# Kernel optimization log

Measured on AMD Instinct MI355X. Metric: run time of the kernel, lower is better.

The kernel has to match this reference:

```python
import jax, jax.numpy as jnp
import numpy as np

H = 32          # total heads
K = 8           # active heads per token
D = 128         # head_dim = embed_dim // active_heads
E = 1024        # embed_dim
S = 1024        # seq_len
MAX_SEQ = 8192
BASE = 10000.0
SCALE = D ** -0.5
LB_W = 0.01
ENT_W = 0.01


def _rope(v, cos, sin):
    # v: (T, D); cos/sin: (T, D)
    v1, v2 = v[:, : D // 2], v[:, D // 2:]
    rot = jnp.concatenate([-v2, v1], axis=-1)
    return v * cos + rot * sin


def setup_inputs() -> dict:
    key = jax.random.key(0)
    ks = jax.random.split(key, 6)
    x = jax.random.normal(ks[0], (1, S, E), jnp.float32)
    Wq = jax.random.normal(ks[1], (E, H * D), jnp.float32) * 0.02
    Wk = jax.random.normal(ks[2], (E, H * D), jnp.float32) * 0.02
    Wv = jax.random.normal(ks[3], (E, H * D), jnp.float32) * 0.02
    Wr = jax.random.normal(ks[4], (E, H), jnp.float32) * 0.02
    Wo = jax.random.normal(ks[5], (K * D, E), jnp.float32) * 0.02
    head_counts = jnp.zeros((1, H), jnp.int32)
    return {"x": x, "Wq": Wq, "Wk": Wk, "Wv": Wv, "Wr": Wr, "Wo": Wo,
            "head_counts": head_counts}


def reference(x, Wq, Wk, Wv, Wr, Wo, head_counts):
    # ---- routing (eval mode: no gumbel noise) ----
    logits = x @ Wr                                   # (1, S, H)
    soft_probs = jax.nn.softmax(logits, axis=-1)
    top_logits, head_idx = jax.lax.top_k(logits, K)   # (1, S, K)
    head_w = jax.nn.softmax(top_logits, axis=-1)      # (1, S, K)

    # ---- aux loss ----
    primary = head_idx[..., 0]                        # (1, S)
    one_hot_p = jax.nn.one_hot(primary, H, dtype=jnp.float32)
    f = one_hot_p.mean(axis=1)                        # (1, H)
    p = soft_probs.mean(axis=1)                       # (1, H)
    balance = H * (f * p).sum(axis=-1).mean()
    entropy = -(soft_probs * jnp.log(soft_probs + 1e-8)).sum(axis=-1)
    entropy_loss = -entropy.mean()
    z_loss = (jax.nn.logsumexp(logits, axis=-1) ** 2).mean() * 0.01
    aux_loss = LB_W * balance + ENT_W * entropy_loss + z_loss

    # ---- projections + per-token gather of selected heads ----
    q_all = (x @ Wq).reshape(1, S, H, D)
    k_all = (x @ Wk).reshape(1, S, H, D)
    v_all = (x @ Wv).reshape(1, S, H, D)
    gidx = head_idx[..., None]                        # (1, S, K, 1)
    q = jnp.take_along_axis(q_all, gidx, axis=2)[0].reshape(S * K, D)
    k = jnp.take_along_axis(k_all, gidx, axis=2)[0].reshape(S * K, D)
    v = jnp.take_along_axis(v_all, gidx, axis=2)[0].reshape(S * K, D)

    heads_flat = head_idx[0].reshape(S * K)           # (T,)

    # rank of each dispatched token within its head (exclusive prefix count)
    oh = jax.nn.one_hot(heads_flat, H, dtype=jnp.int32)   # (T, H)
    excl = jnp.cumsum(oh, axis=0) - oh
    rank = jnp.take_along_axis(excl, heads_flat[:, None], axis=1)[:, 0]
    positions = rank + head_counts[0, heads_flat]
    positions = jnp.clip(positions, 0, MAX_SEQ - 1)

    # ---- per-head RoPE with per-head position counters ----
    inv_freq = 1.0 / (BASE ** (jnp.arange(0, D, 2, dtype=jnp.float32) / D))
    freqs = positions.astype(jnp.float32)[:, None] * inv_freq[None, :]
    emb = jnp.concatenate([freqs, freqs], axis=-1)    # (T, D)
    cos, sin = jnp.cos(emb), jnp.sin(emb)
    q = _rope(q, cos, sin)
    k = _rope(k, cos, sin)

    # ---- block-diagonal-causal attention (same head, earlier dispatch order) ----
    idx = jnp.arange(S * K)
    mask = (heads_flat[:, None] == heads_flat[None, :]) & (idx[None, :] <= idx[:, None])
    scores = (q @ k.T) * SCALE                        # (T, T)
    scores = jnp.where(mask, scores, jnp.float32(-1e30))
    attn = jax.nn.softmax(scores, axis=-1)
    out = attn @ v                                    # (T, D)

    # ---- combine with routing weights + output projection ----
    out = out.reshape(S, K, D) * head_w[0][..., None]
    out = out.reshape(S, K * D) @ Wo                  # (S, E)
    output = out[None]                                # (1, S, E)

    updated_counts = head_counts + oh.sum(axis=0)[None]
    return output, updated_counts, aux_loss
```

## Files before the change

kernel.cpp:

```cpp
#include <hip/hip_runtime.h>
#include <math.h>

#define S 1024
#define E 1024
#define H 32
#define KSEL 8
#define D 128
#define HD 4096
#define SK 8192
#define MAXL 1024
#define CAP 9216
#define ATTN_SCALE 0.08838834764831845f
#define SSTR 36
#define PSTR 40

#define NROUTER 256
#define NCONV 64
#define NTAB 512

typedef _Float16 half8 __attribute__((ext_vector_type(8)));
typedef _Float16 half4 __attribute__((ext_vector_type(4)));
typedef float floatx16 __attribute__((ext_vector_type(16)));
typedef float f4 __attribute__((ext_vector_type(4)));

#define GLOAD_LDS16(gsrc, ldst) \
    __builtin_amdgcn_global_load_lds( \
        (const __attribute__((address_space(1))) void*)(gsrc), \
        (__attribute__((address_space(3))) void*)(ldst), 16, 0, 0)

__global__ __launch_bounds__(256) void router_conv_kernel(
    const float* __restrict__ x, const float* __restrict__ Wr,
    int* __restrict__ head_idx, float* __restrict__ head_w,
    float* __restrict__ pbuf, float* __restrict__ entz,
    _Float16* __restrict__ xh,
    const float* __restrict__ Wo, _Float16* __restrict__ Wot,
    float2* __restrict__ tab)
{
    int bid = blockIdx.x, tid = threadIdx.x;
    if (bid >= NROUTER + NCONV) {
        int base = (bid - NROUTER - NCONV) * 1024;
        #pragma unroll
        for (int j = 0; j < 4; ++j) {
            int idx = base + j * 256 + tid;
            int p = idx >> 6, d2 = idx & 63;
            float inv = exp2f((float)d2 * -0.20762050f);
            float ang = (float)p * inv;
            float sn, cs;
            sincosf(ang, &sn, &cs);
            tab[idx] = make_float2(cs, sn);
        }
        return;
    }
    if (bid >= NROUTER) {
        __shared__ _Float16 tl[128 * 128];
        int cb = bid - NROUTER;
        int c0 = (cb & 7) * 128, r0 = (cb >> 3) * 128;
        #pragma unroll
        for (int p = 0; p < 16; ++p) {
            int idx = p * 256 + tid;
            int rr = idx >> 5, cg = (idx & 31) * 4;
            f4 v = *(const f4*)&Wo[(size_t)(r0 + rr) * 1024 + c0 + cg];
            half4 o;
            o.x = (_Float16)v.x; o.y = (_Float16)v.y;
            o.z = (_Float16)v.z; o.w = (_Float16)v.w;
            int sc = cg ^ (((rr >> 3) & 7) << 2);
            *(half4*)&tl[rr * 128 + sc] = o;
        }
        __syncthreads();
        #pragma unroll
        for (int p = 0; p < 8; ++p) {
            int chunk = p * 256 + tid;
            int cc = chunk >> 4, ch = chunk & 15;
            int cidx = cc ^ ((ch & 7) << 2);
            half8 o;
            #pragma unroll
            for (int j = 0; j < 8; ++j)
                o[j] = tl[(ch * 8 + j) * 128 + cidx];
            *(half8*)&Wot[(size_t)(c0 + cc) * 1024 + r0 + ch * 8] = o;
        }
        return;
    }
    int s = bid * 4 + (tid >> 6);
    int lane = tid & 63;
    int h = lane & 31, half = lane >> 5;
    const float* xr = x + (size_t)s * E + half * 512;
    const float* wr = Wr + (size_t)(half * 512) * H + h;
    float a0 = 0.f, a1 = 0.f, a2 = 0.f, a3 = 0.f;
    #pragma unroll 4
    for (int e = 0; e < 512; e += 4) {
        a0 += xr[e]     * wr[e * H];
        a1 += xr[e + 1] * wr[(e + 1) * H];
        a2 += xr[e + 2] * wr[(e + 2) * H];
        a3 += xr[e + 3] * wr[(e + 3) * H];
    }
    float acc = (a0 + a1) + (a2 + a3);
    acc += __shfl_xor(acc, 32, 64);
    float logit = acc;
    float m = logit;
    #pragma unroll
    for (int off = 16; off; off >>= 1) m = fmaxf(m, __shfl_xor(m, off, 64));
    float ex = expf(logit - m);
    float Z = ex;
    #pragma unroll
    for (int off = 16; off; off >>= 1) Z += __shfl_xor(Z, off, 64);
    float p = ex / Z;
    float es = p * logf(p + 1e-8f);
    #pragma unroll
    for (int off = 16; off; off >>= 1) es += __shfl_xor(es, off, 64);
    float lse = m + logf(Z);
    float lv = logit;
    float tv[KSEL]; int ti[KSEL];
    #pragma unroll
    for (int j = 0; j < KSEL; ++j) {
        float bv = lv; int bi = h;
        #pragma unroll
        for (int off = 16; off; off >>= 1) {
            float ov = __shfl_xor(bv, off, 64);
            int oi = __shfl_xor(bi, off, 64);
            if (ov > bv || (ov == bv && oi < bi)) { bv = ov; bi = oi; }
        }
        tv[j] = bv; ti[j] = bi;
        if (h == bi) lv = -INFINITY;
    }
    float Z2 = 0.f;
    #pragma unroll
    for (int j = 0; j < KSEL; ++j) Z2 += expf(tv[j] - tv[0]);
    if (lane < 32) pbuf[s * 32 + lane] = p;
    if (lane == 0) {
        entz[s * 2]     = es;
        entz[s * 2 + 1] = lse * lse;
        #pragma unroll
        for (int j = 0; j < KSEL; ++j) {
            head_idx[s * KSEL + j] = ti[j];
            head_w[s * KSEL + j]   = expf(tv[j] - tv[0]) / Z2;
        }
    }
    const float* xrow = x + (size_t)s * E;
    _Float16* xhrow = xh + (size_t)s * E;
    #pragma unroll
    for (int t = 0; t < 4; ++t) {
        int e = t * 256 + lane * 4;
        f4 v = *(const f4*)&xrow[e];
        half4 o;
        o.x = (_Float16)v.x; o.y = (_Float16)v.y; o.z = (_Float16)v.z; o.w = (_Float16)v.w;
        *(half4*)&xhrow[e] = o;
    }
}

__global__ __launch_bounds__(256) void scan_aux_kernel(
    const int* __restrict__ head_idx, const int* __restrict__ head_counts,
    int* __restrict__ order, int* __restrict__ hlen, float* __restrict__ out_counts,
    const float* __restrict__ pbuf, const float* __restrict__ entz,
    float* __restrict__ out_aux)
{
    int bid = blockIdx.x, tid = threadIdx.x;
    if (bid == H) {
        int hh = tid & 31, grp = tid >> 5;
        __shared__ float red[256], red2[256];
        __shared__ float psum[32];
        __shared__ int hist[32];
        if (tid < 32) hist[tid] = 0;
        float ps = 0.f;
        for (int s = grp; s < S; s += 8) ps += pbuf[s * 32 + hh];
        red[tid] = ps;
        float es = 0.f, zs = 0.f;
        for (int s = tid; s < S; s += 256) { es += entz[s * 2]; zs += entz[s * 2 + 1]; }
        red2[tid] = es;
        __syncthreads();
        if (grp == 0) {
            float v = 0.f;
            #pragma unroll
            for (int j = 0; j < 8; ++j) v += red[j * 32 + hh];
            psum[hh] = v;
        }
        __syncthreads();
        red[tid] = zs;
        for (int s = tid; s < S; s += 256)
            atomicAdd(&hist[head_idx[s * KSEL]], 1);
        __syncthreads();
        for (int stp = 128; stp; stp >>= 1) {
            if (tid < stp) { red[tid] += red[tid + stp]; red2[tid] += red2[tid + stp]; }
            __syncthreads();
        }
        if (tid == 0) {
            float bal = 0.f;
            for (int j = 0; j < H; ++j)
                bal += ((float)hist[j] / (float)S) * (psum[j] / (float)S);
            bal *= (float)H;
            float ent_loss = red2[0] / (float)S;
            float z = red[0] / (float)S * 0.01f;
            out_aux[0] = 0.01f * bal + 0.01f * ent_loss + z;
        }
        return;
    }
    int h = bid;
    int wave = tid >> 6, lane = tid & 63;
    __shared__ int wtot[4][4];
    int base = 0;
    int hc = head_counts[h];
    int v0 = head_idx[tid],       v1 = head_idx[256 + tid];
    int v2 = head_idx[512 + tid], v3 = head_idx[768 + tid];
    unsigned long long lt = (1ull << lane) - 1ull;
    for (int c0 = 0; c0 < SK; c0 += 1024) {
        int n0 = 0, n1 = 0, n2 = 0, n3 = 0;
        if (c0 + 1024 < SK) {
            n0 = head_idx[c0 + 1024 + tid]; n1 = head_idx[c0 + 1280 + tid];
            n2 = head_idx[c0 + 1536 + tid]; n3 = head_idx[c0 + 1792 + tid];
        }
        bool p0 = (v0 == h), p1 = (v1 == h), p2 = (v2 == h), p3 = (v3 == h);
        unsigned long long m0 = __ballot(p0), m1 = __ballot(p1);
        unsigned long long m2 = __ballot(p2), m3 = __ballot(p3);
        int w0 = __popcll(m0 & lt), w1 = __popcll(m1 & lt);
        int w2 = __popcll(m2 & lt), w3 = __popcll(m3 & lt);
        if (lane == 0) {
            wtot[0][wave] = __popcll(m0); wtot[1][wave] = __popcll(m1);
            wtot[2][wave] = __popcll(m2); wtot[3][wave] = __popcll(m3);
        }
        __syncthreads();
        int pw[4], T[4];
        #pragma unroll
        for (int i = 0; i < 4; ++i) {
            int pre = 0, tot = 0;
            #pragma unroll
            for (int w = 0; w < 4; ++w) {
                int tv = wtot[i][w];
                if (w < wave) pre += tv;
                tot += tv;
            }
            pw[i] = pre; T[i] = tot;
        }
        if (p0) order[h * MAXL + base + pw[0] + w0] = c0 + tid;
        if (p1) order[h * MAXL + base + T[0] + pw[1] + w1] = c0 + 256 + tid;
        if (p2) order[h * MAXL + base + T[0] + T[1] + pw[2] + w2] = c0 + 512 + tid;
        if (p3) order[h * MAXL + base + T[0] + T[1] + T[2] + pw[3] + w3] = c0 + 768 + tid;
        base += T[0] + T[1] + T[2] + T[3];
        __syncthreads();
        v0 = n0; v1 = n1; v2 = n2; v3 = n3;
    }
    if (tid == 0) {
        hlen[h] = base;
        out_counts[h] = (float)(hc + base);
    }
}

__global__ __launch_bounds__(512) void qkv_direct(
    const _Float16* __restrict__ xh,
    const float* __restrict__ Wq, const float* __restrict__ Wk, const float* __restrict__ Wv,
    const int* __restrict__ order, const int* __restrict__ hlen,
    const int* __restrict__ head_counts, const float2* __restrict__ tab,
    _Float16* __restrict__ qh, _Float16* __restrict__ kh, _Float16* __restrict__ vT)
{
    int bid = blockIdx.x;
    int hs = bid & 1;
    int h  = (bid >> 1) & 31;
    int z  = bid >> 6;
    const float* W = (z == 0) ? Wq : (z == 1) ? Wk : Wv;

    int len = hlen[h];
    int hb = 0;
    for (int i = 0; i < h; ++i) hb += (hlen[i] + 31) & ~31;
    int lenp = (len + 31) & ~31;

    int tid = threadIdx.x;
    int wv = tid >> 6;
    int lane = tid & 63;
    int l32 = lane & 31, g = lane >> 5;

    __shared__ _Float16 Bsh[64 * 512];

    int scol = tid & 63;
    int pscol = ((scol >> 5) << 6) + hs * 32 + (scol & 31);
    const float* wcol = W + (size_t)h * D + pscol;

    int npass = (len > 512) ? 2 : 1;
    int tok[2][2];
    #pragma unroll
    for (int p = 0; p < 2; ++p)
        #pragma unroll
        for (int rt = 0; rt < 2; ++rt) {
            int r = p * 512 + wv * 64 + rt * 32 + l32;
            tok[p][rt] = (r < len) ? (order[h * MAXL + r] >> 3) : 0;
        }

    floatx16 acc[2][2][2] = {};

    for (int khf = 0; khf < 2; ++khf) {
        int kbase = khf * 512;
        if (khf) __syncthreads();
        {
            int eg = tid >> 6;
            const float* wp = wcol + (size_t)(kbase + eg * 8) * HD;
            for (int rnd = 0; rnd < 8; ++rnd) {
                float v[8];
                #pragma unroll
                for (int j = 0; j < 8; ++j) v[j] = wp[(size_t)j * HD];
                half8 o;
                #pragma unroll
                for (int j = 0; j < 8; ++j) o[j] = (_Float16)v[j];
                int e0 = rnd * 64 + eg * 8;
                *(half8*)&Bsh[scol * 512 + (e0 ^ ((scol & 7) << 3))] = o;
                wp += (size_t)64 * HD;
            }
        }
        __syncthreads();
        #pragma unroll
        for (int p = 0; p < 2; ++p) {
            if (p < npass) {
                const _Float16* ap0 = xh + (size_t)tok[p][0] * E + kbase + g * 8;
                const _Float16* ap1 = xh + (size_t)tok[p][1] * E + kbase + g * 8;
                #pragma unroll 2
                for (int kb = 0; kb < 8; ++kb) {
                    half8 A0[4], A1[4];
                    #pragma unroll
                    for (int kc = 0; kc < 4; ++kc) {
                        A0[kc] = *(const half8*)(ap0 + kb * 64 + kc * 16);
                        A1[kc] = *(const half8*)(ap1 + kb * 64 + kc * 16);
                    }
                    #pragma unroll
                    for (int kc = 0; kc < 4; ++kc) {
                        int kk = kb * 64 + kc * 16 + g * 8;
                        int kkx = kk ^ ((l32 & 7) << 3);
                        half8 b0 = *(const half8*)&Bsh[l32 * 512 + kkx];
                        half8 b1 = *(const half8*)&Bsh[(32 + l32) * 512 + kkx];
                        acc[p][0][0] = __builtin_amdgcn_mfma_f32_32x32x16_f16(A0[kc], b0, acc[p][0][0], 0, 0, 0);
                        acc[p][0][1] = __builtin_amdgcn_mfma_f32_32x32x16_f16(A0[kc], b1, acc[p][0][1], 0, 0, 0);
                        acc[p][1][0] = __builtin_amdgcn_mfma_f32_32x32x16_f16(A1[kc], b0, acc[p][1][0], 0, 0, 0);
                        acc[p][1][1] = __builtin_amdgcn_mfma_f32_32x32x16_f16(A1[kc], b1, acc[p][1][1], 0, 0, 0);
                    }
                }
            }
        }
    }

    if (z < 2) {
        _Float16* dst = (z == 0) ? qh : kh;
        int hc = head_counts[h];
        int d2 = hs * 32 + l32;
        #pragma unroll
        for (int p = 0; p < 2; ++p) {
            if (p < npass) {
                #pragma unroll
                for (int rt = 0; rt < 2; ++rt) {
                    int base = p * 512 + wv * 64 + rt * 32;
                    #pragma unroll
                    for (int reg = 0; reg < 16; ++reg) {
                        int slot = base + (reg & 3) + 8 * (reg >> 2) + 4 * g;
                        if (slot < len) {
                            int pos = slot + hc;
                            pos = pos < 0 ? 0 : (pos > 8191 ? 8191 : pos);
                            float2 tt = tab[pos * 64 + d2];
                            float v1 = acc[p][rt][0][reg], v2 = acc[p][rt][1][reg];
                            _Float16* dp = dst + ((size_t)hb + slot) * D;
                            dp[d2]      = (_Float16)(v1 * tt.x - v2 * tt.y);
                            dp[d2 + 64] = (_Float16)(v2 * tt.x + v1 * tt.y);
                        }
                    }
                }
            }
        }
    } else {
        #pragma unroll
        for (int p = 0; p < 2; ++p) {
            if (p < npass) {
                #pragma unroll
                for (int rt = 0; rt < 2; ++rt) {
                    int base = p * 512 + wv * 64 + rt * 32;
                    #pragma unroll
                    for (int nf = 0; nf < 2; ++nf) {
                        int pcol = nf * 64 + hs * 32 + l32;
                        _Float16* vp0 = vT + (size_t)hb * D + (size_t)pcol * lenp;
                        #pragma unroll
                        for (int q4 = 0; q4 < 4; ++q4) {
                            int slot0 = base + 8 * q4 + 4 * g;
                            if (slot0 + 3 < len) {
                                half4 o;
                                o.x = (_Float16)acc[p][rt][nf][q4 * 4 + 0];
                                o.y = (_Float16)acc[p][rt][nf][q4 * 4 + 1];
                                o.z = (_Float16)acc[p][rt][nf][q4 * 4 + 2];
                                o.w = (_Float16)acc[p][rt][nf][q4 * 4 + 3];
                                *(half4*)(vp0 + slot0) = o;
                            } else {
                                #pragma unroll
                                for (int r2 = 0; r2 < 4; ++r2) {
                                    int sl = slot0 + r2;
                                    if (sl < len) vp0[sl] = (_Float16)acc[p][rt][nf][q4 * 4 + r2];
                                    else if (sl < lenp) vp0[sl] = (_Float16)0.f;
                                }
                            }
                        }
                    }
                }
            }
        }
    }
}

__global__ __launch_bounds__(128) void attn_mfma(
    const _Float16* __restrict__ qh, const _Float16* __restrict__ kh,
    const _Float16* __restrict__ vT,
    const int* __restrict__ order, const int* __restrict__ hlen,
    const float* __restrict__ head_w, _Float16* __restrict__ ao)
{
    int h = blockIdx.x >> 5, qt = blockIdx.x & 31;
    int len = hlen[h];
    int row0 = qt * 32;
    if (row0 >= len) return;
    int hb = 0;
    for (int i = 0; i < h; ++i) hb += (hlen[i] + 31) & ~31;
    int lenp = (len + 31) & ~31;
    int tid = threadIdx.x;
    int w = tid >> 6, lane = tid & 63;
    int l32 = lane & 31, g = lane >> 5;
    int srow = lane >> 1, shalf = lane & 1;

    __shared__ float Sld[2][32 * SSTR];
    __shared__ _Float16 Pld[2][32 * PSTR];
    __shared__ float alphaLd[2][32];
    __shared__ float mlLd[32][4];
    __shared__ float facLd[32][3];
    __shared__ int flatLd[32];
    __shared__ float Obuf[32][128];

    if (tid < 32) {
        int r = row0 + tid;
        flatLd[tid] = (r < len) ? order[h * MAXL + r] : -1;
    }

    const _Float16* qrow = qh + ((size_t)hb + row0 + l32) * D;
    half8 qf[8];
    #pragma unroll
    for (int t = 0; t < 8; ++t) qf[t] = *(const half8*)(qrow + t * 16 + g * 8);

    floatx16 O[4] = {};
    float m_run = -INFINITY, l_run = 0.f;

    if (w <= qt) {
        half8 kf[8], kfn[8], vv[8];
        {
            const _Float16* krow = kh + ((size_t)hb + w * 32 + l32) * D;
            #pragma unroll
            for (int t = 0; t < 8; ++t) kf[t] = *(const half8*)(krow + t * 16 + g * 8);
        }
        for (int kt = w; kt <= qt; kt += 2) {
            int col0 = kt * 32;
            floatx16 Sc = {};
            #pragma unroll
            for (int t = 0; t < 8; ++t)
                Sc = __builtin_amdgcn_mfma_f32_32x32x16_f16(qf[t], kf[t], Sc, 0, 0, 0);
            #pragma unroll
            for (int nt = 0; nt < 4; ++nt) {
                const _Float16* vp = vT + (size_t)hb * D + (size_t)(nt * 32 + l32) * lenp + col0;
                vv[nt * 2]     = *(const half8*)(vp + g * 8);
                vv[nt * 2 + 1] = *(const half8*)(vp + 16 + g * 8);
            }
            if (kt + 2 <= qt) {
                const _Float16* krow = kh + ((size_t)hb + col0 + 64 + l32) * D;
                #pragma unroll
                for (int t = 0; t < 8; ++t) kfn[t] = *(const half8*)(krow + t * 16 + g * 8);
            }
            bool diag = (kt == qt);
            #pragma unroll
            for (int reg = 0; reg < 16; ++reg) {
                int row = (reg & 3) + 8 * (reg >> 2) + 4 * g;
                float s = Sc[reg] * ATTN_SCALE;
                if (diag && l32 > row) s = -1e30f;
                Sld[w][row * SSTR + l32] = s;
            }
            __builtin_amdgcn_wave_barrier();
            const float* sp = &Sld[w][srow * SSTR + shalf * 16];
            float va[16];
            *(f4*)(va)      = *(const f4*)(sp);
            *(f4*)(va + 4)  = *(const f4*)(sp + 4);
            *(f4*)(va + 8)  = *(const f4*)(sp + 8);
            *(f4*)(va + 12) = *(const f4*)(sp + 12);
            float mt_ = va[0];
            #pragma unroll
            for (int j = 1; j < 16; ++j) mt_ = fmaxf(mt_, va[j]);
            mt_ = fmaxf(mt_, __shfl_xor(mt_, 1, 64));
            float m_new = fmaxf(m_run, mt_);
            float alpha = __expf(m_run - m_new);
            float p[16], tsum = 0.f;
            #pragma unroll
            for (int j = 0; j < 16; ++j) { p[j] = __expf(va[j] - m_new); tsum += p[j]; }
            tsum += __shfl_xor(tsum, 1, 64);
            l_run = l_run * alpha + tsum;
            m_run = m_new;
            half8 ph0, ph1;
            #pragma unroll
            for (int j = 0; j < 8; ++j) { ph0[j] = (_Float16)p[j]; ph1[j] = (_Float16)p[j + 8]; }
            *(half8*)&Pld[w][srow * PSTR + shalf * 16]     = ph0;
            *(half8*)&Pld[w][srow * PSTR + shalf * 16 + 8] = ph1;
            if (shalf == 0) alphaLd[w][srow] = alpha;
            __builtin_amdgcn_wave_barrier();
            f4 al[4];
            #pragma unroll
            for (int qq = 0; qq < 4; ++qq) al[qq] = *(const f4*)&alphaLd[w][4 * g + 8 * qq];
            #pragma unroll
            for (int reg = 0; reg < 16; ++reg) {
                float av = al[reg >> 2][reg & 3];
                O[0][reg] *= av; O[1][reg] *= av; O[2][reg] *= av; O[3][reg] *= av;
            }
            half8 pf0 = *(const half8*)&Pld[w][l32 * PSTR + g * 8];
            half8 pf1 = *(const half8*)&Pld[w][l32 * PSTR + 16 + g * 8];
            #pragma unroll
            for (int nt = 0; nt < 4; ++nt) {
                O[nt] = __builtin_amdgcn_mfma_f32_32x32x16_f16(pf0, vv[nt * 2],     O[nt], 0, 0, 0);
                O[nt] = __builtin_amdgcn_mfma_f32_32x32x16_f16(pf1, vv[nt * 2 + 1], O[nt], 0, 0, 0);
            }
            __builtin_amdgcn_wave_barrier();
            #pragma unroll
            for (int t = 0; t < 8; ++t) kf[t] = kfn[t];
        }
    }
    if (shalf == 0) { mlLd[srow][w * 2] = m_run; mlLd[srow][w * 2 + 1] = l_run; }
    __syncthreads();
    if (tid < 32) {
        float m0 = mlLd[tid][0], l0 = mlLd[tid][1];
        float m1 = mlLd[tid][2], l1 = mlLd[tid][3];
        float ms = fmaxf(m0, m1);
        float f0 = __expf(m0 - ms), f1 = __expf(m1 - ms);
        float lt = f0 * l0 + f1 * l1;
        int flat = flatLd[tid];
        float hw = (flat >= 0) ? head_w[flat] : 0.f;
        facLd[tid][0] = f1;
        facLd[tid][1] = hw / lt;
        facLd[tid][2] = f0;
    }
    __syncthreads();
    if (w == 1) {
        #pragma unroll
        for (int nt = 0; nt < 4; ++nt) {
            int col = nt * 32 + l32;
            #pragma unroll
            for (int reg = 0; reg < 16; ++reg) {
                int row = (reg & 3) + 8 * (reg >> 2) + 4 * g;
                Obuf[row][col] = O[nt][reg] * facLd[row][0];
            }
        }
    }
    __syncthreads();
    if (w == 0) {
        #pragma unroll
        for (int nt = 0; nt < 4; ++nt) {
            int col = nt * 32 + l32;
            #pragma unroll
            for (int reg = 0; reg < 16; ++reg) {
                int row = (reg & 3) + 8 * (reg >> 2) + 4 * g;
                int flat = flatLd[row];
                if (flat >= 0) {
                    float val = (O[nt][reg] * facLd[row][2] + Obuf[row][col]) * facLd[row][1];
                    ao[(size_t)flat * D + col] = (_Float16)val;
                }
            }
        }
    }
}

__global__ __launch_bounds__(256) void out_mfma(
    const _Float16* __restrict__ A, const _Float16* __restrict__ Bt,
    float* __restrict__ C)
{
    int n0 = blockIdx.x * 64, m0 = blockIdx.y * 64;
    int tid = threadIdx.x, wave = tid >> 6, lane = tid & 63;
    int wm = wave >> 1, wn = wave & 1;
    int l32 = lane & 31, g = lane >> 5;

    __shared__ _Float16 Bs[2][64 * 64];

    const _Float16* aptr = A + (size_t)(m0 + wm * 32 + l32) * 1024;

    auto stageB = [&](int buf, int k0) {
        #pragma unroll
        for (int it = 0; it < 2; ++it) {
            int f = it * 256 + tid;
            int row = f >> 3, c = f & 7;
            int sc = c ^ (row & 7);
            GLOAD_LDS16(Bt + (size_t)(n0 + row) * 1024 + k0 + sc * 8, &Bs[buf][f * 8]);
        }
    };

    floatx16 acc = {};
    int brow = wn * 32 + l32;
    half8 a_cur[4], a_nxt[4];
    #pragma unroll
    for (int ks = 0; ks < 4; ++ks)
        a_cur[ks] = *(const half8*)(aptr + ks * 16 + g * 8);

    auto compute = [&](int buf, half8* a) {
        #pragma unroll
        for (int ks = 0; ks < 4; ++ks) {
            int wchunk = ks * 2 + g;
            half8 bf = *(const half8*)&Bs[buf][brow * 64 + (wchunk ^ (brow & 7)) * 8];
            acc = __builtin_amdgcn_mfma_f32_32x32x16_f16(a[ks], bf, acc, 0, 0, 0);
        }
    };

    stageB(0, 0);
    __syncthreads();
    int buf = 0;
    for (int k0 = 64; k0 < 1024; k0 += 64) {
        stageB(buf ^ 1, k0);
        #pragma unroll
        for (int ks = 0; ks < 4; ++ks)
            a_nxt[ks] = *(const half8*)(aptr + k0 + ks * 16 + g * 8);
        compute(buf, a_cur);
        __syncthreads();
        buf ^= 1;
        #pragma unroll
        for (int ks = 0; ks < 4; ++ks) a_cur[ks] = a_nxt[ks];
    }
    compute(buf, a_cur);

    int col = n0 + wn * 32 + l32;
    #pragma unroll
    for (int reg = 0; reg < 16; ++reg) {
        int row = m0 + wm * 32 + (reg & 3) + 8 * (reg >> 2) + 4 * g;
        C[(size_t)row * 1024 + col] = acc[reg];
    }
}

extern "C" void kernel_launch(void* const* d_in, const int* in_sizes, int n_in,
                              void* d_out, int out_size, void* d_ws, size_t ws_size,
                              hipStream_t stream)
{
    const float* x  = (const float*)d_in[0];
    const float* Wq = (const float*)d_in[1];
    const float* Wk = (const float*)d_in[2];
    const float* Wv = (const float*)d_in[3];
    const float* Wr = (const float*)d_in[4];
    const float* Wo = (const float*)d_in[5];
    const int* head_counts = (const int*)d_in[6];
    float* out = (float*)d_out;

    float* head_w = (float*)d_ws;
    float* pbuf   = head_w + SK;
    float* entz   = pbuf + S * 32;
    int* head_idx = (int*)(entz + S * 2);
    int* order    = head_idx + SK;
    int* hlen     = order + H * MAXL;
    _Float16* xh   = (_Float16*)(hlen + 64);
    _Float16* aoh  = xh + (size_t)S * E;
    _Float16* Wot  = aoh + (size_t)SK * D;
    _Float16* qh   = Wot + (size_t)1024 * 1024;
    _Float16* kh   = qh + (size_t)CAP * D;
    _Float16* vT   = kh + (size_t)CAP * D;
    float2* tab    = (float2*)(vT + (size_t)CAP * D);

    router_conv_kernel<<<NROUTER + NCONV + NTAB, 256, 0, stream>>>(
        x, Wr, head_idx, head_w, pbuf, entz, xh, Wo, Wot, tab);
    scan_aux_kernel<<<33, 256, 0, stream>>>(head_idx, head_counts, order, hlen,
                                            out + (size_t)S * E, pbuf, entz,
                                            out + (size_t)S * E + H);
    qkv_direct<<<192, 512, 0, stream>>>(xh, Wq, Wk, Wv, order, hlen, head_counts, tab,
                                        qh, kh, vT);
    attn_mfma<<<H * 32, 128, 0, stream>>>(qh, kh, vT, order, hlen, head_w, aoh);
    out_mfma<<<dim3(16, 16), 256, 0, stream>>>(aoh, Wot, out);
}
```

Measured before the change: 222.1 us.

## Stage weight panels via direct global-to-LDS loads in smaller K chunks

The projection kernel used to load fp32 weight columns with strided scalar global loads, one row per load, convert them to fp16 and write them into a 512-wide shared panel. It now issues 16-byte global-to-LDS loads (GLOAD_LDS16) into an fp32 staging buffer, converts from LDS into a 256-wide swizzled fp16 panel, and walks K in four 256-chunks instead of two 512-chunks. The aim is more coalesced, wider weight fetches that bypass registers. In exchange it adds a 32 KB fp32 staging buffer and more barriers per K step, which raises LDS use and may lower occupancy.

```diff
diff --git a/kernel.cpp b/kernel.cpp
--- a/kernel.cpp
+++ b/kernel.cpp
@@ -266,11 +266,14 @@
     int lane = tid & 63;
     int l32 = lane & 31, g = lane >> 5;
 
-    __shared__ _Float16 Bsh[64 * 512];
-
-    int scol = tid & 63;
-    int pscol = ((scol >> 5) << 6) + hs * 32 + (scol & 31);
-    const float* wcol = W + (size_t)h * D + pscol;
+    __shared__ _Float16 Bsh[64 * 256];
+    __shared__ __align__(16) float Sf[8192];
+
+    int chunkl = lane & 15;
+    int grpc = chunkl >> 3;
+    int pcol = grpc * 64 + hs * 32 + (chunkl & 7) * 4;
+    int rowin = lane >> 4;
+    const float* Wbase = W + (size_t)h * D + pcol;
 
     int npass = (len > 512) ? 2 : 1;
     int tok[2][2];
@@ -284,32 +287,37 @@
 
     floatx16 acc[2][2][2] = {};
 
-    for (int khf = 0; khf < 2; ++khf) {
-        int kbase = khf * 512;
-        if (khf) __syncthreads();
-        {
-            int eg = tid >> 6;
-            const float* wp = wcol + (size_t)(kbase + eg * 8) * HD;
-            for (int rnd = 0; rnd < 8; ++rnd) {
-                float v[8];
-                #pragma unroll
-                for (int j = 0; j < 8; ++j) v[j] = wp[(size_t)j * HD];
+    for (int q = 0; q < 4; ++q) {
+        int kq = q * 256;
+        for (int c = 0; c < 2; ++c) {
+            int kc0 = kq + c * 128;
+            #pragma unroll
+            for (int j = 0; j < 4; ++j) {
+                int instr = wv * 4 + j;
+                const float* src = Wbase + (size_t)(kc0 + instr * 4 + rowin) * HD;
+                GLOAD_LDS16(src, &Sf[instr * 256]);
+            }
+            __syncthreads();
+            #pragma unroll
+            for (int halfk = 0; halfk < 2; ++halfk) {
                 half8 o;
                 #pragma unroll
-                for (int j = 0; j < 8; ++j) o[j] = (_Float16)v[j];
-                int e0 = rnd * 64 + eg * 8;
-                *(half8*)&Bsh[scol * 512 + (e0 ^ ((scol & 7) << 3))] = o;
-                wp += (size_t)64 * HD;
-            }
-        }
-        __syncthreads();
+                for (int j2 = 0; j2 < 8; ++j2) {
+                    int kk = wv * 16 + halfk * 8 + j2;
+                    o[j2] = (_Float16)Sf[kk * 64 + lane];
+                }
+                int kpan = c * 128 + wv * 16 + halfk * 8;
+                *(half8*)&Bsh[lane * 256 + (kpan ^ ((lane & 7) << 3))] = o;
+            }
+            __syncthreads();
+        }
         #pragma unroll
         for (int p = 0; p < 2; ++p) {
             if (p < npass) {
-                const _Float16* ap0 = xh + (size_t)tok[p][0] * E + kbase + g * 8;
-                const _Float16* ap1 = xh + (size_t)tok[p][1] * E + kbase + g * 8;
+                const _Float16* ap0 = xh + (size_t)tok[p][0] * E + kq + g * 8;
+                const _Float16* ap1 = xh + (size_t)tok[p][1] * E + kq + g * 8;
                 #pragma unroll 2
-                for (int kb = 0; kb < 8; ++kb) {
+                for (int kb = 0; kb < 4; ++kb) {
                     half8 A0[4], A1[4];
                     #pragma unroll
                     for (int kc = 0; kc < 4; ++kc) {
@@ -320,8 +328,8 @@
                     for (int kc = 0; kc < 4; ++kc) {
                         int kk = kb * 64 + kc * 16 + g * 8;
                         int kkx = kk ^ ((l32 & 7) << 3);
-                        half8 b0 = *(const half8*)&Bsh[l32 * 512 + kkx];
-                        half8 b1 = *(const half8*)&Bsh[(32 + l32) * 512 + kkx];
+                        half8 b0 = *(const half8*)&Bsh[l32 * 256 + kkx];
+                        half8 b1 = *(const half8*)&Bsh[(32 + l32) * 256 + kkx];
                         acc[p][0][0] = __builtin_amdgcn_mfma_f32_32x32x16_f16(A0[kc], b0, acc[p][0][0], 0, 0, 0);
                         acc[p][0][1] = __builtin_amdgcn_mfma_f32_32x32x16_f16(A0[kc], b1, acc[p][0][1], 0, 0, 0);
                         acc[p][1][0] = __builtin_amdgcn_mfma_f32_32x32x16_f16(A1[kc], b0, acc[p][1][0], 0, 0, 0);
@@ -367,8 +375,8 @@
                     int base = p * 512 + wv * 64 + rt * 32;
                     #pragma unroll
                     for (int nf = 0; nf < 2; ++nf) {
-                        int pcol = nf * 64 + hs * 32 + l32;
-                        _Float16* vp0 = vT + (size_t)hb * D + (size_t)pcol * lenp;
+                        int pcolo = nf * 64 + hs * 32 + l32;
+                        _Float16* vp0 = vT + (size_t)hb * D + (size_t)pcolo * lenp;
                         #pragma unroll
                         for (int q4 = 0; q4 < 4; ++q4) {
                             int slot0 = base + 8 * q4 + 4 * g;
```

Result: no change. 225.8 us (+1.7%).
